# Kernel tuning notes

Hardware: AMD Instinct MI355X
Metric: run time of the kernel (lower is better)

## Reference

```python
import jax, jax.numpy as jnp
import numpy as np

N_TOKENS = 2097152
N_FEATURES = 64
N_MODELS = 64
N_LAYERS = 4


def setup_inputs() -> dict:
    key = jax.random.key(0)
    k1, k2, k3 = jax.random.split(key, 3)
    x = jax.random.normal(k1, (N_TOKENS, N_FEATURES), dtype=jnp.float32)
    # Packed per-model Linear params, torch convention: weight [out, in]
    scale = 1.0 / np.sqrt(N_FEATURES)
    W = jax.random.normal(k2, (N_MODELS, N_LAYERS, N_FEATURES, N_FEATURES), dtype=jnp.float32) * scale
    b = jax.random.normal(k3, (N_MODELS, N_LAYERS, N_FEATURES), dtype=jnp.float32) * scale
    return {"x": x, "W": W, "b": b}


def reference(x, W, b):
    # x: [N, d]; rows are partitioned into N_MODELS equal contiguous slices.
    # W: [M, L, d_out, d_in], b: [M, L, d_out]
    n, d = x.shape
    xg = x.reshape(N_MODELS, n // N_MODELS, d)  # [M, n_per, d]
    for l in range(N_LAYERS):
        # torch Linear: y = x @ W.T + b, per model (grouped GEMM)
        xg = jnp.einsum('mnd,mfd->mnf', xg, W[:, l]) + b[:, l][:, None, :]
        xg = jax.nn.relu(xg)
    return xg.reshape(n, d)
```

## Files before the change

### kernel.cpp

```cpp
#include <hip/hip_runtime.h>


typedef __attribute__((ext_vector_type(8))) _Float16 f16x8;
typedef __attribute__((ext_vector_type(2))) __fp16 fp16x2;
typedef __attribute__((ext_vector_type(4))) float f32x4;

#define MODELS 64
#define LAYERS 4
#define DIM 64
#define TOKS_PER_MODEL 32768
#define BLOCKS_PER_MODEL 16
#define WAVES_PER_BLOCK 4
#define WAVES_PER_MODEL (BLOCKS_PER_MODEL * WAVES_PER_BLOCK)
#define STEPS 32
#define STEP_FLOATS ((size_t)WAVES_PER_MODEL * 16 * DIM)

#define WF_BYTES (LAYERS * 4 * 2 * 64 * 16)
#define BIAS_OFF WF_BYTES
#define LDS_BYTES (WF_BYTES + LAYERS * DIM * 4)

union H8 { f16x8 v; fp16x2 h2[4]; };

__global__ __launch_bounds__(256, 2) void mlp4_fused(
    const float* __restrict__ x, const float* __restrict__ W,
    const float* __restrict__ b, float* __restrict__ out) {

    __shared__ __align__(16) unsigned char smem[LDS_BYTES];

    const int lane = threadIdx.x & 63;
    const int wave = threadIdx.x >> 6;
    const int c = lane & 15;
    const int g = lane >> 4;

    const int m   = blockIdx.x / BLOCKS_PER_MODEL;
    const int blk = blockIdx.x % BLOCKS_PER_MODEL;
    const int q   = blk * WAVES_PER_BLOCK + wave;

    {
        const int l = wave;
        const float* Wl = W + ((size_t)m * LAYERS + l) * DIM * DIM;
        #pragma unroll
        for (int t = 0; t < 4; ++t) {
            const float* row = Wl + (size_t)(t * 16 + c) * DIM + 4 * g;
            f32x4 c0 = *(const f32x4*)(row + 0);
            f32x4 c1 = *(const f32x4*)(row + 16);
            f32x4 c2 = *(const f32x4*)(row + 32);
            f32x4 c3 = *(const f32x4*)(row + 48);
            H8 a0, a1;
            #pragma unroll
            for (int e = 0; e < 4; ++e) {
                a0.v[e]     = (_Float16)c0[e];
                a0.v[4 + e] = (_Float16)c1[e];
                a1.v[e]     = (_Float16)c2[e];
                a1.v[4 + e] = (_Float16)c3[e];
            }
            *(f16x8*)(smem + ((size_t)((l * 4 + t) * 2 + 0) * 1024) + lane * 16) = a0.v;
            *(f16x8*)(smem + ((size_t)((l * 4 + t) * 2 + 1) * 1024) + lane * 16) = a1.v;
        }
        if (lane < 16) {
            const float* bl = b + ((size_t)m * LAYERS + l) * DIM + lane * 4;
            *(f32x4*)(smem + BIAS_OFF + l * 256 + lane * 16) = *(const f32x4*)bl;
        }
    }
    __syncthreads();

    const float* xp = x   + ((size_t)m * TOKS_PER_MODEL + (size_t)q * 16) * DIM
                          + (size_t)(c * DIM + 4 * g);
    float*       op = out + ((size_t)m * TOKS_PER_MODEL + (size_t)q * 16) * DIM
                          + (size_t)(c * DIM + 4 * g);

    f32x4 xr0 = *(const f32x4*)(xp + 0);
    f32x4 xr1 = *(const f32x4*)(xp + 16);
    f32x4 xr2 = *(const f32x4*)(xp + 32);
    f32x4 xr3 = *(const f32x4*)(xp + 48);

    #pragma unroll 1
    for (int s = 0; s < STEPS; ++s) {
        const int nxt = (s + 1) & (STEPS - 1);
        const float* nx = xp + (size_t)nxt * STEP_FLOATS;
        f32x4 xn0 = *(const f32x4*)(nx + 0);
        f32x4 xn1 = *(const f32x4*)(nx + 16);
        f32x4 xn2 = *(const f32x4*)(nx + 32);
        f32x4 xn3 = *(const f32x4*)(nx + 48);

        H8 z0u, z1u;
        z0u.h2[0] = __builtin_amdgcn_cvt_pkrtz(xr0[0], xr0[1]);
        z0u.h2[1] = __builtin_amdgcn_cvt_pkrtz(xr0[2], xr0[3]);
        z0u.h2[2] = __builtin_amdgcn_cvt_pkrtz(xr1[0], xr1[1]);
        z0u.h2[3] = __builtin_amdgcn_cvt_pkrtz(xr1[2], xr1[3]);
        z1u.h2[0] = __builtin_amdgcn_cvt_pkrtz(xr2[0], xr2[1]);
        z1u.h2[1] = __builtin_amdgcn_cvt_pkrtz(xr2[2], xr2[3]);
        z1u.h2[2] = __builtin_amdgcn_cvt_pkrtz(xr3[0], xr3[1]);
        z1u.h2[3] = __builtin_amdgcn_cvt_pkrtz(xr3[2], xr3[3]);
        f16x8 z0 = z0u.v, z1 = z1u.v;

        f32x4 acc[4];
        #pragma unroll
        for (int l = 0; l < LAYERS; ++l) {
            #pragma unroll
            for (int t = 0; t < 4; ++t)
                acc[t] = *(const f32x4*)(smem + BIAS_OFF + l * 256 + t * 64 + g * 16);
            #pragma unroll
            for (int t = 0; t < 4; ++t) {
                f16x8 w0 = *(const f16x8*)(smem + ((size_t)((l * 4 + t) * 2 + 0) * 1024) + lane * 16);
                acc[t] = __builtin_amdgcn_mfma_f32_16x16x32_f16(w0, z0, acc[t], 0, 0, 0);
            }
            #pragma unroll
            for (int t = 0; t < 4; ++t) {
                f16x8 w1 = *(const f16x8*)(smem + ((size_t)((l * 4 + t) * 2 + 1) * 1024) + lane * 16);
                acc[t] = __builtin_amdgcn_mfma_f32_16x16x32_f16(w1, z1, acc[t], 0, 0, 0);
            }

            if (l < LAYERS - 1) {
                H8 n0, n1;
                #pragma unroll
                for (int t = 0; t < 2; ++t) {
                    n0.h2[t * 2 + 0] = __builtin_amdgcn_cvt_pkrtz(
                        fmaxf(acc[t][0], 0.0f), fmaxf(acc[t][1], 0.0f));
                    n0.h2[t * 2 + 1] = __builtin_amdgcn_cvt_pkrtz(
                        fmaxf(acc[t][2], 0.0f), fmaxf(acc[t][3], 0.0f));
                    n1.h2[t * 2 + 0] = __builtin_amdgcn_cvt_pkrtz(
                        fmaxf(acc[2 + t][0], 0.0f), fmaxf(acc[2 + t][1], 0.0f));
                    n1.h2[t * 2 + 1] = __builtin_amdgcn_cvt_pkrtz(
                        fmaxf(acc[2 + t][2], 0.0f), fmaxf(acc[2 + t][3], 0.0f));
                }
                z0 = n0.v;
                z1 = n1.v;
            }
        }

        float* o = op + (size_t)s * STEP_FLOATS;
        #pragma unroll
        for (int t = 0; t < 4; ++t) {
            f32x4 res;
            #pragma unroll
            for (int r = 0; r < 4; ++r) res[r] = fmaxf(acc[t][r], 0.0f);
            *(f32x4*)(o + t * 16) = res;
        }

        xr0 = xn0; xr1 = xn1; xr2 = xn2; xr3 = xn3;
    }
}

extern "C" void kernel_launch(void* const* d_in, const int* in_sizes, int n_in,
                              void* d_out, int out_size, void* d_ws, size_t ws_size,
                              hipStream_t stream) {
    (void)in_sizes; (void)n_in; (void)out_size; (void)d_ws; (void)ws_size;
    const float* x = (const float*)d_in[0];
    const float* W = (const float*)d_in[1];
    const float* b = (const float*)d_in[2];
    float* out = (float*)d_out;
    mlp4_fused<<<dim3(MODELS * BLOCKS_PER_MODEL), dim3(256), 0, stream>>>(x, W, b, out);
}
```

Before: 228.4 us.

## Stage x tiles through LDS via async global_load_lds and coalesce output stores

Replaces direct per-lane strided register loads of x with double-buffered global_load_lds DMA into a swizzled per-wave LDS buffer, then reads MFMA fragments from LDS. Outputs are written back into the same LDS buffer and re-read in a row-contiguous layout so global stores become fully coalesced 1KB segments. Biases move from LDS into registers packed as bf16, which reduces LDS traffic but rounds the bias to bf16 precision. This adds LDS usage and waitcnt synchronization, and the bf16 bias rounding risks accuracy.

```diff
diff --git a/kernel.cpp b/kernel.cpp
--- a/kernel.cpp
+++ b/kernel.cpp
@@ -11,15 +11,41 @@
 #define TOKS_PER_MODEL 32768
 #define BLOCKS_PER_MODEL 16
 #define WAVES_PER_BLOCK 4
-#define WAVES_PER_MODEL (BLOCKS_PER_MODEL * WAVES_PER_BLOCK)
+#define WAVES_PER_MODEL 64
 #define STEPS 32
 #define STEP_FLOATS ((size_t)WAVES_PER_MODEL * 16 * DIM)
+#define STEP_BYTES (STEP_FLOATS * 4)
 
 #define WF_BYTES (LAYERS * 4 * 2 * 64 * 16)
-#define BIAS_OFF WF_BYTES
-#define LDS_BYTES (WF_BYTES + LAYERS * DIM * 4)
+#define XBUF_OFF WF_BYTES
+#define LDS_BYTES (WF_BYTES + WAVES_PER_BLOCK * 2 * 4096)
 
 union H8 { f16x8 v; fp16x2 h2[4]; };
+
+static __device__ __forceinline__ unsigned bf16bits(float f) {
+    unsigned u = __builtin_bit_cast(unsigned, f);
+    return (u + 0x7fffu + ((u >> 16) & 1u)) >> 16;
+}
+
+static __device__ __forceinline__ void dma16(const void* g, void* l) {
+    __builtin_amdgcn_global_load_lds(
+        (const __attribute__((address_space(1))) unsigned int*)g,
+        (__attribute__((address_space(3))) unsigned int*)l, 16, 0, 0);
+}
+
+#define CVT_Z(Z0, Z1, X0, X1, X2, X3)                              \
+    {                                                              \
+        H8 z0u_, z1u_;                                             \
+        z0u_.h2[0] = __builtin_amdgcn_cvt_pkrtz(X0[0], X0[1]);     \
+        z0u_.h2[1] = __builtin_amdgcn_cvt_pkrtz(X0[2], X0[3]);     \
+        z0u_.h2[2] = __builtin_amdgcn_cvt_pkrtz(X1[0], X1[1]);     \
+        z0u_.h2[3] = __builtin_amdgcn_cvt_pkrtz(X1[2], X1[3]);     \
+        z1u_.h2[0] = __builtin_amdgcn_cvt_pkrtz(X2[0], X2[1]);     \
+        z1u_.h2[1] = __builtin_amdgcn_cvt_pkrtz(X2[2], X2[3]);     \
+        z1u_.h2[2] = __builtin_amdgcn_cvt_pkrtz(X3[0], X3[1]);     \
+        z1u_.h2[3] = __builtin_amdgcn_cvt_pkrtz(X3[2], X3[3]);     \
+        Z0 = z0u_.v; Z1 = z1u_.v;                                  \
+    }
 
 __global__ __launch_bounds__(256, 2) void mlp4_fused(
     const float* __restrict__ x, const float* __restrict__ W,
@@ -57,49 +83,80 @@
             *(f16x8*)(smem + ((size_t)((l * 4 + t) * 2 + 0) * 1024) + lane * 16) = a0.v;
             *(f16x8*)(smem + ((size_t)((l * 4 + t) * 2 + 1) * 1024) + lane * 16) = a1.v;
         }
-        if (lane < 16) {
-            const float* bl = b + ((size_t)m * LAYERS + l) * DIM + lane * 4;
-            *(f32x4*)(smem + BIAS_OFF + l * 256 + lane * 16) = *(const f32x4*)bl;
-        }
+    }
+
+    unsigned bpk[LAYERS][8];
+    {
+        const float* bm = b + (size_t)m * LAYERS * DIM;
+        #pragma unroll
+        for (int l = 0; l < LAYERS; ++l)
+            #pragma unroll
+            for (int t = 0; t < 4; ++t)
+                #pragma unroll
+                for (int p2 = 0; p2 < 2; ++p2) {
+                    unsigned r0 = bf16bits(bm[l * DIM + t * 16 + 4 * g + 2 * p2]);
+                    unsigned r1 = bf16bits(bm[l * DIM + t * 16 + 4 * g + 2 * p2 + 1]);
+                    bpk[l][t * 2 + p2] = (r1 << 16) | r0;
+                }
     }
     __syncthreads();
 
-    const float* xp = x   + ((size_t)m * TOKS_PER_MODEL + (size_t)q * 16) * DIM
-                          + (size_t)(c * DIM + 4 * g);
-    float*       op = out + ((size_t)m * TOKS_PER_MODEL + (size_t)q * 16) * DIM
-                          + (size_t)(c * DIM + 4 * g);
-
-    f32x4 xr0 = *(const f32x4*)(xp + 0);
-    f32x4 xr1 = *(const f32x4*)(xp + 16);
-    f32x4 xr2 = *(const f32x4*)(xp + 32);
-    f32x4 xr3 = *(const f32x4*)(xp + 48);
-
+    int frOff[4];
+    #pragma unroll
+    for (int t = 0; t < 4; ++t)
+        frOff[t] = (c * 256 + t * 64 + g * 16) ^ ((c & 7) << 4);
+
+    int srcOff[4], brOff[4];
+    #pragma unroll
+    for (int kk = 0; kk < 4; ++kk) {
+        const int cc = kk * 4 + (lane >> 4);
+        const int u  = lane & 15;
+        const int v  = (u & 8) | ((u & 7) ^ (cc & 7));
+        srcOff[kk] = cc * 256 + (v >> 2) * 64 + (v & 3) * 16;
+        brOff[kk]  = (kk * 1024 + lane * 16) ^ ((cc & 7) << 4);
+    }
+
+    const char* xTile = (const char*)(x + ((size_t)m * TOKS_PER_MODEL + (size_t)q * 16) * DIM);
+    char*       oBase = (char*)(out + ((size_t)m * TOKS_PER_MODEL + (size_t)q * 16) * DIM) + lane * 16;
+    unsigned char* xb = smem + XBUF_OFF + wave * 8192;
+
+    #pragma unroll
+    for (int kk = 0; kk < 4; ++kk)
+        dma16(xTile + srcOff[kk], xb + kk * 1024);
+    asm volatile("s_waitcnt vmcnt(0)" ::: "memory");
+
+    int p = 0;
     #pragma unroll 1
     for (int s = 0; s < STEPS; ++s) {
-        const int nxt = (s + 1) & (STEPS - 1);
-        const float* nx = xp + (size_t)nxt * STEP_FLOATS;
-        f32x4 xn0 = *(const f32x4*)(nx + 0);
-        f32x4 xn1 = *(const f32x4*)(nx + 16);
-        f32x4 xn2 = *(const f32x4*)(nx + 32);
-        f32x4 xn3 = *(const f32x4*)(nx + 48);
-
-        H8 z0u, z1u;
-        z0u.h2[0] = __builtin_amdgcn_cvt_pkrtz(xr0[0], xr0[1]);
-        z0u.h2[1] = __builtin_amdgcn_cvt_pkrtz(xr0[2], xr0[3]);
-        z0u.h2[2] = __builtin_amdgcn_cvt_pkrtz(xr1[0], xr1[1]);
-        z0u.h2[3] = __builtin_amdgcn_cvt_pkrtz(xr1[2], xr1[3]);
-        z1u.h2[0] = __builtin_amdgcn_cvt_pkrtz(xr2[0], xr2[1]);
-        z1u.h2[1] = __builtin_amdgcn_cvt_pkrtz(xr2[2], xr2[3]);
-        z1u.h2[2] = __builtin_amdgcn_cvt_pkrtz(xr3[0], xr3[1]);
-        z1u.h2[3] = __builtin_amdgcn_cvt_pkrtz(xr3[2], xr3[3]);
-        f16x8 z0 = z0u.v, z1 = z1u.v;
+        unsigned char* bufc = xb + p * 4096;
+
+        f32x4 X0 = *(const f32x4*)(bufc + frOff[0]);
+        f32x4 X1 = *(const f32x4*)(bufc + frOff[1]);
+        f32x4 X2 = *(const f32x4*)(bufc + frOff[2]);
+        f32x4 X3 = *(const f32x4*)(bufc + frOff[3]);
+
+        {
+            const size_t ns = (size_t)((s + 1) & (STEPS - 1)) * STEP_BYTES;
+            unsigned char* nb = xb + (p ^ 1) * 4096;
+            #pragma unroll
+            for (int kk = 0; kk < 4; ++kk)
+                dma16(xTile + ns + srcOff[kk], nb + kk * 1024);
+        }
+
+        f16x8 z0, z1;
+        CVT_Z(z0, z1, X0, X1, X2, X3);
 
         f32x4 acc[4];
         #pragma unroll
         for (int l = 0; l < LAYERS; ++l) {
             #pragma unroll
-            for (int t = 0; t < 4; ++t)
-                acc[t] = *(const f32x4*)(smem + BIAS_OFF + l * 256 + t * 64 + g * 16);
+            for (int t = 0; t < 4; ++t) {
+                unsigned p0 = bpk[l][t * 2], p1 = bpk[l][t * 2 + 1];
+                acc[t][0] = __builtin_bit_cast(float, p0 << 16);
+                acc[t][1] = __builtin_bit_cast(float, p0 & 0xffff0000u);
+                acc[t][2] = __builtin_bit_cast(float, p1 << 16);
+                acc[t][3] = __builtin_bit_cast(float, p1 & 0xffff0000u);
+            }
             #pragma unroll
             for (int t = 0; t < 4; ++t) {
                 f16x8 w0 = *(const f16x8*)(smem + ((size_t)((l * 4 + t) * 2 + 0) * 1024) + lane * 16);
@@ -110,7 +167,6 @@
                 f16x8 w1 = *(const f16x8*)(smem + ((size_t)((l * 4 + t) * 2 + 1) * 1024) + lane * 16);
                 acc[t] = __builtin_amdgcn_mfma_f32_16x16x32_f16(w1, z1, acc[t], 0, 0, 0);
             }
-
             if (l < LAYERS - 1) {
                 H8 n0, n1;
                 #pragma unroll
@@ -129,16 +185,30 @@
             }
         }
 
-        float* o = op + (size_t)s * STEP_FLOATS;
         #pragma unroll
         for (int t = 0; t < 4; ++t) {
             f32x4 res;
             #pragma unroll
             for (int r = 0; r < 4; ++r) res[r] = fmaxf(acc[t][r], 0.0f);
-            *(f32x4*)(o + t * 16) = res;
-        }
-
-        xr0 = xn0; xr1 = xn1; xr2 = xn2; xr3 = xn3;
+            *(f32x4*)(bufc + frOff[t]) = res;
+        }
+        asm volatile("s_waitcnt lgkmcnt(0)" ::: "memory");
+        __builtin_amdgcn_sched_barrier(0);
+
+        {
+            char* o = oBase + (size_t)s * STEP_BYTES;
+            f32x4 O0 = *(const f32x4*)(bufc + brOff[0]);
+            f32x4 O1 = *(const f32x4*)(bufc + brOff[1]);
+            f32x4 O2 = *(const f32x4*)(bufc + brOff[2]);
+            f32x4 O3 = *(const f32x4*)(bufc + brOff[3]);
+            *(f32x4*)(o + 0)    = O0;
+            *(f32x4*)(o + 1024) = O1;
+            *(f32x4*)(o + 2048) = O2;
+            *(f32x4*)(o + 3072) = O3;
+        }
+
+        asm volatile("s_waitcnt vmcnt(4)" ::: "memory");
+        p ^= 1;
     }
 }
 
```

Result: faster. 220.0 us (-3.7%).
